# Optimization experiments

Hardware: AMD Instinct MI355X
Metric: run time of the kernel (lower is better)

The kernel has to match this reference:

```python
import jax, jax.numpy as jnp
import numpy as np

B, C_IN, C_OUT, N, T, K = 64, 64, 64, 22, 1024, 3


def setup_inputs() -> dict:
    key = jax.random.key(0)
    ks = jax.random.split(key, 6)
    return {
        "x": jax.random.normal(ks[0], (B, C_IN, N, T), dtype=jnp.float32),
        "adj_param": jax.random.normal(ks[1], (N, N), dtype=jnp.float32),
        # ChebConv: K Linear(in,out,bias=False) weights + one shared bias
        "cheb_weight": jax.random.normal(ks[2], (K, C_IN, C_OUT), dtype=jnp.float32) / np.float32(np.sqrt(C_IN)),
        "cheb_bias": jnp.zeros((C_OUT,), dtype=jnp.float32),
        # Conv2d(out, out, kernel=(N,1))
        "agg_weight": jax.random.normal(ks[3], (C_OUT, C_OUT, N, 1), dtype=jnp.float32) / np.float32(np.sqrt(C_OUT * N)),
        "agg_bias": jnp.zeros((C_OUT,), dtype=jnp.float32),
    }


def _forward(x, adj_param, cheb_weight, cheb_bias, agg_weight, agg_bias):
    b, c_in, n, t = x.shape
    k_order = cheb_weight.shape[0]
    # dynamic adjacency: sigmoid, symmetrize, zero diagonal
    adj = jax.nn.sigmoid(adj_param)
    adj = (adj + adj.T) * 0.5
    adj = adj * (1.0 - jnp.eye(n, dtype=adj.dtype))
    # ChebConv scaled Laplacian with lambda_max=2 (PyG default):
    # L_hat = 2/lambda_max * (I - D^-1/2 A D^-1/2) - I = -D^-1/2 A D^-1/2
    deg = jnp.sum(adj, axis=1)
    dis = 1.0 / jnp.sqrt(deg)  # all degrees > 0 since sigmoid > 0
    s = -(dis[:, None] * adj * dis[None, :])  # [N, N], symmetric
    # [B, T, N, C] layout matching x.permute(0,3,2,1)
    xt = jnp.transpose(x, (0, 3, 2, 1))
    # Chebyshev recursion: T0=x, T1=S x, Tk = 2 S T(k-1) - T(k-2)
    tx0 = xt
    out = jnp.einsum('btnc,co->btno', tx0, cheb_weight[0])
    tx1 = jnp.einsum('vn,btnc->btvc', s, tx0)
    out = out + jnp.einsum('btnc,co->btno', tx1, cheb_weight[1])
    for k in range(2, k_order):
        tx2 = 2.0 * jnp.einsum('vn,btnc->btvc', s, tx1) - tx0
        out = out + jnp.einsum('btnc,co->btno', tx2, cheb_weight[k])
        tx0, tx1 = tx1, tx2
    out = out + cheb_bias
    # back to [B, O, N, T]
    out = jnp.transpose(out, (0, 3, 2, 1))
    # Conv2d with kernel (N,1): contract channels and nodes -> [B, O, 1, T]
    out = jnp.einsum('bcnt,ocn->bot', out, agg_weight[..., 0]) + agg_bias[None, :, None]
    return out[:, :, None, :]


def reference(x, adj_param, cheb_weight, cheb_bias, agg_weight, agg_bias):
    return _forward(x, adj_param, cheb_weight, cheb_bias, agg_weight, agg_bias)
```

## Files before the change

### kernel.cpp

```cpp
#include <hip/hip_runtime.h>
#include <hip/hip_bf16.h>

#define B_    64
#define C_    64
#define N_    22
#define T_    1024
#define O_    64
#define KTOT  1408
#define KSTEPS 44

typedef __bf16 bf16x8 __attribute__((ext_vector_type(8)));
typedef float  f32x4  __attribute__((ext_vector_type(4)));

typedef __attribute__((address_space(1))) float f32_g;
typedef __attribute__((address_space(3))) float f32_l;

__global__ __launch_bounds__(256) void prep_all(
    const float* __restrict__ adjp,
    const float* __restrict__ chebw,
    const float* __restrict__ chebb,
    const float* __restrict__ aggw,
    const float* __restrict__ aggb,
    __bf16* __restrict__ Mfrag,
    float* __restrict__ constv)
{
    const int o   = blockIdx.x >> 2;
    const int kq  = blockIdx.x & 3;
    const int tid = threadIdx.x;
    __shared__ float sm[484];
    __shared__ float c2[484];
    __shared__ float dis[22];
    __shared__ float aggs[KTOT];
    __shared__ float F1[KTOT];
    __shared__ float F2[KTOT];
    __shared__ float red[256];

    for (int e = tid; e < 484; e += 256) {
        int i = e / 22, j = e - i * 22;
        float a = 0.5f * (1.f / (1.f + expf(-adjp[i * 22 + j])) +
                          1.f / (1.f + expf(-adjp[j * 22 + i])));
        c2[e] = (i == j) ? 0.f : a;
    }
    for (int e = tid; e < KTOT; e += 256) aggs[e] = aggw[o * KTOT + e];
    __syncthreads();
    if (tid < 22) {
        float d = 0.f;
        for (int n = 0; n < 22; ++n) d += c2[tid * 22 + n];
        dis[tid] = rsqrtf(d);
    }
    __syncthreads();
    for (int e = tid; e < 484; e += 256) {
        int i = e / 22, j = e - i * 22;
        sm[e] = -dis[i] * c2[e] * dis[j];
    }
    __syncthreads();
    for (int e = tid; e < 484; e += 256) {
        int i = e / 22, j = e - i * 22;
        float acc = 0.f;
        for (int n = 0; n < 22; ++n) acc += sm[i * 22 + n] * sm[n * 22 + j];
        c2[e] = 2.f * acc - (i == j ? 1.f : 0.f);
    }
    __syncthreads();
    for (int e = tid; e < KTOT; e += 256) {
        int cp = e / 22, v = e - cp * 22;
        float a1 = 0.f, a2 = 0.f;
        for (int n = 0; n < 22; ++n) {
            float w = aggs[cp * 22 + n];
            a1 += w * sm[n * 22 + v];
            a2 += w * c2[n * 22 + v];
        }
        F1[e] = a1;
        F2[e] = a2;
    }
    if (kq == 0) {
        float p = 0.f;
        for (int e = tid; e < KTOT; e += 256) p += aggs[e] * chebb[e / 22];
        red[tid] = p;
    }
    __syncthreads();
    if (kq == 0) {
#pragma unroll
        for (int st = 128; st > 0; st >>= 1) {
            if (tid < st) red[tid] += red[tid + st];
            __syncthreads();
        }
        if (tid == 0) constv[o] = red[0] + aggb[o];
    }

    const int fo = o >> 4, l15 = o & 15;
    const int kend = (kq + 1) * 352;
    for (int k = kq * 352 + tid; k < kend; k += 256) {
        int c = k / 22, v = k - c * 22;
        const float* w0 = chebw + c * 64;
        float a0 = 0.f, a1 = 0.f, a2 = 0.f;
        for (int cp = 0; cp < 64; ++cp) {
            int idx = cp * 22 + v;
            a0 += w0[cp] * aggs[idx];
            a1 += w0[4096 + cp] * F1[idx];
            a2 += w0[8192 + cp] * F2[idx];
        }
        int ks = k >> 5, r = k & 31, lhi = r >> 3, j = r & 7;
        Mfrag[(((ks * 4 + fo) * 64) + lhi * 16 + l15) * 8 + j] = (__bf16)(a0 + a1 + a2);
    }
}

#define WAITV(N) asm volatile("s_waitcnt vmcnt(" #N ")" ::: "memory")
#define BARR do { __builtin_amdgcn_s_barrier(); __builtin_amdgcn_sched_barrier(0); } while (0)

__global__ __launch_bounds__(512, 2) void gemm_main(
    const float* __restrict__ x,
    const __bf16* __restrict__ Mfrag,
    const float* __restrict__ constv,
    float* __restrict__ y)
{
    __shared__ float lds[3 * 8192];

    const int bid  = ((blockIdx.x & 7) << 5) | (blockIdx.x >> 3);
    const int b    = bid >> 2;
    const int tq   = bid & 3;
    const int wave = threadIdx.x >> 6;
    const int lane = threadIdx.x & 63;
    const int tcol = lane & 15;
    const int kg   = lane >> 4;

    const size_t xbase = (size_t)b * ((size_t)KTOT * T_) + (size_t)tq * 256;

    const int rd0 = (kg * 8) * 256 + ((((wave << 1) | 0) ^ (kg & 1)) << 4) + tcol;
    const int rd1 = (kg * 8) * 256 + ((((wave << 1) | 1) ^ (kg & 1)) << 4) + tcol;

    const __bf16* mf = Mfrag + (size_t)lane * 8;

    f32x4 acc[2][4];
#pragma unroll
    for (int m = 0; m < 2; ++m)
#pragma unroll
        for (int fo = 0; fo < 4; ++fo) acc[m][fo] = (f32x4){0.f, 0.f, 0.f, 0.f};

    auto STAGE = [&](int ks, float* buf) {
#pragma unroll
        for (int q = 0; q < 4; ++q) {
            const int r = wave * 4 + q;
            const int s = (r >> 3) & 1;
            const int g = ((lane >> 2) ^ s);
            const float* src = x + xbase + (size_t)(ks * 32 + r) * T_
                             + g * 16 + (lane & 3) * 4;
            float* dst = buf + r * 256;
            __builtin_amdgcn_global_load_lds((const f32_g*)src, (f32_l*)dst, 16, 0, 18);
        }
    };
    auto PREFA = [&](bf16x8* dst, int ks) {
        const __bf16* p = mf + (size_t)ks * 2048;
#pragma unroll
        for (int fo = 0; fo < 4; ++fo)
            dst[fo] = *reinterpret_cast<const bf16x8*>(p + fo * 512);
    };
    auto COMPUTE = [&](const bf16x8* a, const float* buf) {
#pragma unroll
        for (int m = 0; m < 2; ++m) {
            const int rb = m ? rd1 : rd0;
            float v[8];
#pragma unroll
            for (int j = 0; j < 8; ++j) v[j] = buf[rb + j * 256];
            bf16x8 bx;
#pragma unroll
            for (int j = 0; j < 8; ++j) bx[j] = (__bf16)v[j];
#pragma unroll
            for (int fo = 0; fo < 4; ++fo)
                acc[m][fo] = __builtin_amdgcn_mfma_f32_16x16x32_bf16(a[fo], bx, acc[m][fo], 0, 0, 0);
        }
    };

    float* const b0 = lds;
    float* const b1 = lds + 8192;
    float* const b2 = lds + 16384;
    bf16x8 ac[4], an[4];

    STAGE(0, b0);
    PREFA(ac, 0);
    STAGE(1, b1);

    for (int i = 0; i < 42; i += 6) {
        WAITV(4); BARR; PREFA(an, i + 1); STAGE(i + 2, b2); COMPUTE(ac, b0);
        WAITV(4); BARR; PREFA(ac, i + 2); STAGE(i + 3, b0); COMPUTE(an, b1);
        WAITV(4); BARR; PREFA(an, i + 3); STAGE(i + 4, b1); COMPUTE(ac, b2);
        WAITV(4); BARR; PREFA(ac, i + 4); STAGE(i + 5, b2); COMPUTE(an, b0);
        WAITV(4); BARR; PREFA(an, i + 5); STAGE(i + 6, b0); COMPUTE(ac, b1);
        WAITV(4); BARR; PREFA(ac, i + 6); STAGE(i + 7, b1); COMPUTE(an, b2);
    }

    WAITV(4); BARR; PREFA(an, 43); COMPUTE(ac, b0);
    WAITV(0); BARR; COMPUTE(an, b1);

    float* yp = y + (size_t)b * (O_ * T_) + tq * 256 + wave * 32 + tcol;
#pragma unroll
    for (int m = 0; m < 2; ++m)
#pragma unroll
        for (int fo = 0; fo < 4; ++fo)
#pragma unroll
            for (int rr = 0; rr < 4; ++rr) {
                int o = fo * 16 + kg * 4 + rr;
                __builtin_nontemporal_store(acc[m][fo][rr] + constv[o],
                                            yp + (size_t)o * T_ + m * 16);
            }
}

extern "C" void kernel_launch(void* const* d_in, const int* in_sizes, int n_in,
                              void* d_out, int out_size, void* d_ws, size_t ws_size,
                              hipStream_t stream)
{
    (void)in_sizes; (void)n_in; (void)out_size; (void)ws_size;
    const float* x     = (const float*)d_in[0];
    const float* adjp  = (const float*)d_in[1];
    const float* chebw = (const float*)d_in[2];
    const float* chebb = (const float*)d_in[3];
    const float* aggw  = (const float*)d_in[4];
    const float* aggb  = (const float*)d_in[5];
    float* y = (float*)d_out;

    char* ws = (char*)d_ws;
    float*  constv = (float*)(ws);
    __bf16* Mfrag  = (__bf16*)(ws + 4096);

    hipLaunchKernelGGL(prep_all, dim3(256), dim3(256), 0, stream,
                       adjp, chebw, chebb, aggw, aggb, Mfrag, constv);
    hipLaunchKernelGGL(gemm_main, dim3(256), dim3(512), 0, stream,
                       x, Mfrag, constv, y);
}
```

Baseline: 78.80 us.

## Fuse weight-prep and GEMM into one cooperative kernel with grid sync

Merges the weight-folding prep kernel and the main GEMM kernel into a single cooperative launch. Each block issues its first two x tile loads, runs its share of the prep work using the third LDS buffer as scratch, then waits on a grid-wide sync before the GEMM loop. The goal is to remove the second launch and its gap and to overlap the first x loads with prep compute. In exchange it adds a grid barrier and the cost of a cooperative launch, and falls back to the two-kernel path if the cooperative launch fails.

```diff
diff --git a/kernel.cpp b/kernel.cpp
--- a/kernel.cpp
+++ b/kernel.cpp
@@ -1,5 +1,8 @@
 #include <hip/hip_runtime.h>
 #include <hip/hip_bf16.h>
+#include <hip/hip_cooperative_groups.h>
+
+namespace cg = cooperative_groups;
 
 #define B_    64
 #define C_    64
@@ -14,6 +17,192 @@
 
 typedef __attribute__((address_space(1))) float f32_g;
 typedef __attribute__((address_space(3))) float f32_l;
+
+#define WAITV(N) asm volatile("s_waitcnt vmcnt(" #N ")" ::: "memory")
+#define BARR do { __builtin_amdgcn_s_barrier(); __builtin_amdgcn_sched_barrier(0); } while (0)
+
+__global__ __launch_bounds__(512, 2) void fused_main(
+    const float* __restrict__ x,
+    const float* __restrict__ adjp,
+    const float* __restrict__ chebw,
+    const float* __restrict__ chebb,
+    const float* __restrict__ aggw,
+    const float* __restrict__ aggb,
+    __bf16* __restrict__ Mfrag,
+    float* __restrict__ constv,
+    float* __restrict__ y)
+{
+    __shared__ float lds[3 * 8192];
+
+    const int tid  = threadIdx.x;
+    const int bid  = ((blockIdx.x & 7) << 5) | (blockIdx.x >> 3);
+    const int b    = bid >> 2;
+    const int tq   = bid & 3;
+    const int wave = tid >> 6;
+    const int lane = tid & 63;
+    const int tcol = lane & 15;
+    const int kg   = lane >> 4;
+
+    const size_t xbase = (size_t)b * ((size_t)KTOT * T_) + (size_t)tq * 256;
+
+    float* const b0 = lds;
+    float* const b1 = lds + 8192;
+    float* const b2 = lds + 16384;
+
+    auto STAGE = [&](int ks, float* buf) {
+#pragma unroll
+        for (int q = 0; q < 4; ++q) {
+            const int r = wave * 4 + q;
+            const int s = (r >> 3) & 1;
+            const int g = ((lane >> 2) ^ s);
+            const float* src = x + xbase + (size_t)(ks * 32 + r) * T_
+                             + g * 16 + (lane & 3) * 4;
+            float* dst = buf + r * 256;
+            __builtin_amdgcn_global_load_lds((const f32_g*)src, (f32_l*)dst, 16, 0, 18);
+        }
+    };
+
+    STAGE(0, b0);
+    STAGE(1, b1);
+
+    {
+        const int po = blockIdx.x >> 2;
+        const int kq = blockIdx.x & 3;
+        float* smv  = b2;
+        float* cm2  = b2 + 484;
+        float* disv = b2 + 968;
+        float* aggs = b2 + 992;
+        float* F1   = b2 + 2400;
+        float* F2   = b2 + 3808;
+        float* red  = b2 + 5216;
+
+        for (int e = tid; e < 484; e += 512) {
+            int i = e / 22, j = e - i * 22;
+            float a = 0.5f * (1.f / (1.f + expf(-adjp[i * 22 + j])) +
+                              1.f / (1.f + expf(-adjp[j * 22 + i])));
+            cm2[e] = (i == j) ? 0.f : a;
+        }
+        for (int e = tid; e < KTOT; e += 512) aggs[e] = aggw[po * KTOT + e];
+        __syncthreads();
+        if (tid < 22) {
+            float d = 0.f;
+            for (int n = 0; n < 22; ++n) d += cm2[tid * 22 + n];
+            disv[tid] = rsqrtf(d);
+        }
+        __syncthreads();
+        for (int e = tid; e < 484; e += 512) {
+            int i = e / 22, j = e - i * 22;
+            smv[e] = -disv[i] * cm2[e] * disv[j];
+        }
+        __syncthreads();
+        for (int e = tid; e < 484; e += 512) {
+            int i = e / 22, j = e - i * 22;
+            float a2 = 0.f;
+            for (int n = 0; n < 22; ++n) a2 += smv[i * 22 + n] * smv[n * 22 + j];
+            cm2[e] = 2.f * a2 - (i == j ? 1.f : 0.f);
+        }
+        __syncthreads();
+        for (int e = tid; e < KTOT; e += 512) {
+            int cp = e / 22, v = e - cp * 22;
+            float a1 = 0.f, a2 = 0.f;
+            for (int n = 0; n < 22; ++n) {
+                float w = aggs[cp * 22 + n];
+                a1 += w * smv[n * 22 + v];
+                a2 += w * cm2[n * 22 + v];
+            }
+            F1[e] = a1;
+            F2[e] = a2;
+        }
+        if (kq == 0) {
+            float p = 0.f;
+            for (int e = tid; e < KTOT; e += 512) p += aggs[e] * chebb[e / 22];
+            red[tid] = p;
+        }
+        __syncthreads();
+        if (kq == 0) {
+            for (int st = 256; st > 0; st >>= 1) {
+                if (tid < st) red[tid] += red[tid + st];
+                __syncthreads();
+            }
+            if (tid == 0) constv[po] = red[0] + aggb[po];
+        }
+        const int pfo = po >> 4, l15 = po & 15;
+        const int kend = (kq + 1) * 352;
+        for (int k = kq * 352 + tid; k < kend; k += 512) {
+            int c = k / 22, v = k - c * 22;
+            const float* w0 = chebw + c * 64;
+            float a0 = 0.f, a1 = 0.f, a2 = 0.f;
+            for (int cp = 0; cp < 64; ++cp) {
+                int idx = cp * 22 + v;
+                a0 += w0[cp] * aggs[idx];
+                a1 += w0[4096 + cp] * F1[idx];
+                a2 += w0[8192 + cp] * F2[idx];
+            }
+            int ks = k >> 5, r = k & 31, lhi = r >> 3, jj = r & 7;
+            Mfrag[(((ks * 4 + pfo) * 64) + lhi * 16 + l15) * 8 + jj] = (__bf16)(a0 + a1 + a2);
+        }
+    }
+
+    cg::this_grid().sync();
+
+    const int rd0 = (kg * 8) * 256 + ((((wave << 1) | 0) ^ (kg & 1)) << 4) + tcol;
+    const int rd1 = (kg * 8) * 256 + ((((wave << 1) | 1) ^ (kg & 1)) << 4) + tcol;
+    const __bf16* mf = Mfrag + (size_t)lane * 8;
+
+    f32x4 acc[2][4];
+#pragma unroll
+    for (int m = 0; m < 2; ++m)
+#pragma unroll
+        for (int fo = 0; fo < 4; ++fo) acc[m][fo] = (f32x4){0.f, 0.f, 0.f, 0.f};
+
+    auto PREFA = [&](bf16x8* dst, int ks) {
+        const __bf16* p = mf + (size_t)ks * 2048;
+#pragma unroll
+        for (int fo = 0; fo < 4; ++fo)
+            dst[fo] = *reinterpret_cast<const bf16x8*>(p + fo * 512);
+    };
+    auto COMPUTE = [&](const bf16x8* a, const float* buf) {
+#pragma unroll
+        for (int m = 0; m < 2; ++m) {
+            const int rb = m ? rd1 : rd0;
+            float v[8];
+#pragma unroll
+            for (int j = 0; j < 8; ++j) v[j] = buf[rb + j * 256];
+            bf16x8 bx;
+#pragma unroll
+            for (int j = 0; j < 8; ++j) bx[j] = (__bf16)v[j];
+#pragma unroll
+            for (int fo = 0; fo < 4; ++fo)
+                acc[m][fo] = __builtin_amdgcn_mfma_f32_16x16x32_bf16(a[fo], bx, acc[m][fo], 0, 0, 0);
+        }
+    };
+
+    bf16x8 ac[4], an[4];
+    PREFA(ac, 0);
+
+    for (int i = 0; i < 42; i += 6) {
+        WAITV(4); BARR; PREFA(an, i + 1); STAGE(i + 2, b2); COMPUTE(ac, b0);
+        WAITV(4); BARR; PREFA(ac, i + 2); STAGE(i + 3, b0); COMPUTE(an, b1);
+        WAITV(4); BARR; PREFA(an, i + 3); STAGE(i + 4, b1); COMPUTE(ac, b2);
+        WAITV(4); BARR; PREFA(ac, i + 4); STAGE(i + 5, b2); COMPUTE(an, b0);
+        WAITV(4); BARR; PREFA(an, i + 5); STAGE(i + 6, b0); COMPUTE(ac, b1);
+        WAITV(4); BARR; PREFA(ac, i + 6); STAGE(i + 7, b1); COMPUTE(an, b2);
+    }
+    WAITV(4); BARR; PREFA(an, 43); COMPUTE(ac, b0);
+    WAITV(0); BARR; COMPUTE(an, b1);
+
+    float* yp = y + (size_t)b * (O_ * T_) + tq * 256 + wave * 32 + tcol;
+#pragma unroll
+    for (int m = 0; m < 2; ++m)
+#pragma unroll
+        for (int fo = 0; fo < 4; ++fo)
+#pragma unroll
+            for (int rr = 0; rr < 4; ++rr) {
+                int o = fo * 16 + kg * 4 + rr;
+                __builtin_nontemporal_store(acc[m][fo][rr] + constv[o],
+                                            yp + (size_t)o * T_ + m * 16);
+            }
+}
 
 __global__ __launch_bounds__(256) void prep_all(
     const float* __restrict__ adjp,
@@ -86,7 +275,6 @@
         }
         if (tid == 0) constv[o] = red[0] + aggb[o];
     }
-
     const int fo = o >> 4, l15 = o & 15;
     const int kend = (kq + 1) * 352;
     for (int k = kq * 352 + tid; k < kend; k += 256) {
@@ -104,9 +292,6 @@
     }
 }
 
-#define WAITV(N) asm volatile("s_waitcnt vmcnt(" #N ")" ::: "memory")
-#define BARR do { __builtin_amdgcn_s_barrier(); __builtin_amdgcn_sched_barrier(0); } while (0)
-
 __global__ __launch_bounds__(512, 2) void gemm_main(
     const float* __restrict__ x,
     const __bf16* __restrict__ Mfrag,
@@ -124,10 +309,8 @@
     const int kg   = lane >> 4;
 
     const size_t xbase = (size_t)b * ((size_t)KTOT * T_) + (size_t)tq * 256;
-
     const int rd0 = (kg * 8) * 256 + ((((wave << 1) | 0) ^ (kg & 1)) << 4) + tcol;
     const int rd1 = (kg * 8) * 256 + ((((wave << 1) | 1) ^ (kg & 1)) << 4) + tcol;
-
     const __bf16* mf = Mfrag + (size_t)lane * 8;
 
     f32x4 acc[2][4];
@@ -187,7 +370,6 @@
         WAITV(4); BARR; PREFA(an, i + 5); STAGE(i + 6, b0); COMPUTE(ac, b1);
         WAITV(4); BARR; PREFA(ac, i + 6); STAGE(i + 7, b1); COMPUTE(an, b2);
     }
-
     WAITV(4); BARR; PREFA(an, 43); COMPUTE(ac, b0);
     WAITV(0); BARR; COMPUTE(an, b1);
 
@@ -221,8 +403,16 @@
     float*  constv = (float*)(ws);
     __bf16* Mfrag  = (__bf16*)(ws + 4096);
 
-    hipLaunchKernelGGL(prep_all, dim3(256), dim3(256), 0, stream,
-                       adjp, chebw, chebb, aggw, aggb, Mfrag, constv);
-    hipLaunchKernelGGL(gemm_main, dim3(256), dim3(512), 0, stream,
-                       x, Mfrag, constv, y);
+    void* args[] = {(void*)&x, (void*)&adjp, (void*)&chebw, (void*)&chebb,
+                    (void*)&aggw, (void*)&aggb, (void*)&Mfrag, (void*)&constv,
+                    (void*)&y};
+    hipError_t err = hipLaunchCooperativeKernel((const void*)fused_main,
+                                                dim3(256), dim3(512),
+                                                args, 0, stream);
+    if (err != hipSuccess) {
+        hipLaunchKernelGGL(prep_all, dim3(256), dim3(256), 0, stream,
+                           adjp, chebw, chebb, aggw, aggb, Mfrag, constv);
+        hipLaunchKernelGGL(gemm_main, dim3(256), dim3(512), 0, stream,
+                           x, Mfrag, constv, y);
+    }
 }
```

After: 116.4 us. 1.48x slower.
